# Performance work log

Hardware: AMD Instinct MI355X
Metric: run time of the kernel (lower is better)

Reference implementation:

```python
import jax, jax.numpy as jnp
import numpy as np

N, E, G, L = 100000, 1600000, 2000, 2000
IN, H1, H2, H3, OUT = 128, 64, 32, 16, 16
EPS = 1e-5


def _layernorm(x, g, b):
    m = jnp.mean(x, axis=-1, keepdims=True)
    v = jnp.mean(jnp.square(x - m), axis=-1, keepdims=True)
    return (x - m) * jax.lax.rsqrt(v + EPS) * g + b


def _gcn_block(x, W, b, Wr, br, g, beta, src, dst, deg_inv_sqrt):
    # GCNConv with added self-loops and symmetric normalization (PyG default)
    h = x @ W  # [N, F]
    coef = (deg_inv_sqrt[src] * deg_inv_sqrt[dst])[:, None]  # [E, 1]
    msg = h[src] * coef  # [E, F] -- dominant memory traffic
    agg = jax.ops.segment_sum(msg, dst, num_segments=N)
    agg = agg + h * jnp.square(deg_inv_sqrt)[:, None] + b  # self-loop term + bias
    out = agg + (x @ Wr + br)  # residual projection
    return jax.nn.relu(_layernorm(out, g, beta))


def setup_inputs():
    key = jax.random.key(0)
    ks = jax.random.split(key, 40)
    w = lambda k, i, o: jax.random.normal(k, (i, o), jnp.float32) / np.sqrt(i)
    d = {}
    d['x'] = jax.random.normal(ks[0], (N, IN), jnp.float32)
    d['src'] = jax.random.randint(ks[1], (E,), 0, N, jnp.int32)
    d['dst'] = jax.random.randint(ks[2], (E,), 0, N, jnp.int32)
    d['batch'] = jnp.sort(jax.random.randint(ks[3], (N,), 0, G, jnp.int32))
    d['link_idx'] = jax.random.randint(ks[4], (2, L), 0, G, jnp.int32)
    dims = [(IN, H1), (H1, H2), (H2, H3), (H3, OUT)]
    for i, (fi, fo) in enumerate(dims, 1):
        d[f'W{i}'] = w(ks[5 + 4 * i], fi, fo)
        d[f'b{i}'] = jnp.zeros((fo,), jnp.float32)
        d[f'Wr{i}'] = w(ks[6 + 4 * i], fi, fo)
        d[f'br{i}'] = jnp.zeros((fo,), jnp.float32)
        d[f'g{i}'] = jnp.ones((fo,), jnp.float32)
        d[f'bt{i}'] = jnp.zeros((fo,), jnp.float32)
    d['Wm1'] = w(ks[30], 2 * OUT, OUT)
    d['bm1'] = jnp.zeros((OUT,), jnp.float32)
    d['Wm2'] = w(ks[31], OUT, OUT // 2)
    d['bm2'] = jnp.zeros((OUT // 2,), jnp.float32)
    d['Wm3'] = w(ks[32], OUT // 2, 1)
    d['bm3'] = jnp.zeros((1,), jnp.float32)
    return d


def reference(x, src, dst, batch, link_idx,
              W1, b1, Wr1, br1, g1, bt1,
              W2, b2, Wr2, br2, g2, bt2,
              W3, b3, Wr3, br3, g3, bt3,
              W4, b4, Wr4, br4, g4, bt4,
              Wm1, bm1, Wm2, bm2, Wm3, bm3):
    ones_e = jnp.ones((E,), jnp.float32)
    deg = jax.ops.segment_sum(ones_e, dst, num_segments=N) + 1.0  # + self-loop
    dis = jax.lax.rsqrt(deg)
    h = _gcn_block(x, W1, b1, Wr1, br1, g1, bt1, src, dst, dis)
    h = _gcn_block(h, W2, b2, Wr2, br2, g2, bt2, src, dst, dis)
    h = _gcn_block(h, W3, b3, Wr3, br3, g3, bt3, src, dst, dis)
    h = _gcn_block(h, W4, b4, Wr4, br4, g4, bt4, src, dst, dis)
    # global mean pool over subgraphs
    cnt = jax.ops.segment_sum(jnp.ones((N,), jnp.float32), batch, num_segments=G)
    gemb = jax.ops.segment_sum(h, batch, num_segments=G) / jnp.maximum(cnt, 1.0)[:, None]
    feat = jnp.concatenate([gemb[link_idx[0]], gemb[link_idx[1]]], axis=1)  # [L, 2*OUT]
    z = jax.nn.relu(feat @ Wm1 + bm1)
    z = jax.nn.relu(z @ Wm2 + bm2)
    z = z @ Wm3 + bm3
    return jax.nn.sigmoid(z).squeeze(-1)  # [L]
```

## Files before the change

### kernel.cpp

```cpp
#include <hip/hip_runtime.h>
#include <math.h>

namespace {

constexpr int N = 100000;
constexpr int E = 1600000;
constexpr int G = 2000;
constexpr int L = 2000;

constexpr int SCAN_CHUNK = 1024;
constexpr int NB = (N + SCAN_CHUNK - 1) / SCAN_CHUNK;

constexpr int NXCD = 8;
constexpr int NP = N / NXCD;

__device__ __forceinline__ float bf2f(unsigned short u) {
  union { unsigned int i; float f; } v;
  v.i = ((unsigned int)u) << 16;
  return v.f;
}
__device__ __forceinline__ unsigned short f2bf(float f) {
  union { float f; unsigned int i; } v;
  v.f = f;
  const unsigned int x = v.i;
  return (unsigned short)((x + 0x7FFFu + ((x >> 16) & 1u)) >> 16);
}


__global__ void hist_part_kernel(const int* __restrict__ dst, int* __restrict__ deg) {
  const int part = blockIdx.x & (NXCD - 1);
  const int lo = part * NP;
  const int hi = lo + NP;
  const int bidp = blockIdx.x >> 3;
  const int stridev = (gridDim.x >> 3) * blockDim.x;
  const int nvec = E >> 2;
  for (int v = bidp * blockDim.x + threadIdx.x; v < nvec; v += stridev) {
    const int4 d4 = *reinterpret_cast<const int4*>(dst + v * 4);
    if (d4.x >= lo && d4.x < hi) atomicAdd(&deg[d4.x], 1);
    if (d4.y >= lo && d4.y < hi) atomicAdd(&deg[d4.y], 1);
    if (d4.z >= lo && d4.z < hi) atomicAdd(&deg[d4.z], 1);
    if (d4.w >= lo && d4.w < hi) atomicAdd(&deg[d4.w], 1);
  }
}

__global__ void fill_part_kernel(const int* __restrict__ src, const int* __restrict__ dst,
                                 int* __restrict__ cursor, int* __restrict__ col) {
  const int part = blockIdx.x & (NXCD - 1);
  const int lo = part * NP;
  const int hi = lo + NP;
  const int bidp = blockIdx.x >> 3;
  const int stridev = (gridDim.x >> 3) * blockDim.x;
  const int nvec = E >> 2;
  for (int v = bidp * blockDim.x + threadIdx.x; v < nvec; v += stridev) {
    const int e = v * 4;
    const int4 d4 = *reinterpret_cast<const int4*>(dst + e);
    if (d4.x >= lo && d4.x < hi) col[atomicAdd(&cursor[d4.x], 1)] = src[e];
    if (d4.y >= lo && d4.y < hi) col[atomicAdd(&cursor[d4.y], 1)] = src[e + 1];
    if (d4.z >= lo && d4.z < hi) col[atomicAdd(&cursor[d4.z], 1)] = src[e + 2];
    if (d4.w >= lo && d4.w < hi) col[atomicAdd(&cursor[d4.w], 1)] = src[e + 3];
  }
}

__global__ void scan1_kernel(const int* __restrict__ deg, int* __restrict__ bsum) {
  const int t = threadIdx.x;
  const int base = blockIdx.x * SCAN_CHUNK + t * 4;
  int s = 0;
  if (base < N) {
    const int4 v = *reinterpret_cast<const int4*>(deg + base);
    s = v.x + v.y + v.z + v.w;
  }
  __shared__ int ss[256];
  ss[t] = s;
  __syncthreads();
#pragma unroll
  for (int off = 128; off >= 1; off >>= 1) {
    if (t < off) ss[t] += ss[t + off];
    __syncthreads();
  }
  if (t == 0) bsum[blockIdx.x] = ss[0];
}

__global__ void scan2_kernel(const int* __restrict__ bsum, int* __restrict__ boff) {
  __shared__ int ss[128];
  const int t = threadIdx.x;
  ss[t] = (t < NB) ? bsum[t] : 0;
  __syncthreads();
#pragma unroll
  for (int off = 1; off < 128; off <<= 1) {
    int v = (t >= off) ? ss[t - off] : 0;
    __syncthreads();
    ss[t] += v;
    __syncthreads();
  }
  if (t < NB) boff[t] = (t == 0) ? 0 : ss[t - 1];
}

__global__ void scan3_kernel(const int* __restrict__ deg, const int* __restrict__ boff,
                             int* __restrict__ row_ptr, int* __restrict__ cursor,
                             float* __restrict__ dis) {
  const int t = threadIdx.x;
  const int base = blockIdx.x * SCAN_CHUNK + t * 4;
  int d0 = 0, d1 = 0, d2 = 0, d3 = 0;
  if (base < N) {
    const int4 v = *reinterpret_cast<const int4*>(deg + base);
    d0 = v.x; d1 = v.y; d2 = v.z; d3 = v.w;
  }
  const int tsum = d0 + d1 + d2 + d3;
  __shared__ int ss[256];
  ss[t] = tsum;
  __syncthreads();
#pragma unroll
  for (int off = 1; off < 256; off <<= 1) {
    int v = (t >= off) ? ss[t - off] : 0;
    __syncthreads();
    ss[t] += v;
    __syncthreads();
  }
  if (base < N) {
    const int p0 = ((t == 0) ? 0 : ss[t - 1]) + boff[blockIdx.x];
    const int p1 = p0 + d0;
    const int p2 = p1 + d1;
    const int p3 = p2 + d2;
    *reinterpret_cast<int4*>(row_ptr + base) = make_int4(p0, p1, p2, p3);
    *reinterpret_cast<int4*>(cursor + base) = make_int4(p0, p1, p2, p3);
    const float4 dv = make_float4(rsqrtf((float)d0 + 1.0f), rsqrtf((float)d1 + 1.0f),
                                  rsqrtf((float)d2 + 1.0f), rsqrtf((float)d3 + 1.0f));
    *reinterpret_cast<float4*>(dis + base) = dv;
  }
  if (blockIdx.x == 0 && t == 0) row_ptr[N] = E;
}


__device__ __forceinline__ void f4fma(float4& a, float s, const float4 w) {
  a.x = fmaf(s, w.x, a.x);
  a.y = fmaf(s, w.y, a.y);
  a.z = fmaf(s, w.z, a.z);
  a.w = fmaf(s, w.w, a.w);
}

template <int FI, int FO>
__global__ __launch_bounds__(1024) void gemm2_kernel(const float* __restrict__ x,
                                                     const float* __restrict__ W,
                                                     const float* __restrict__ Wr,
                                                     const float* __restrict__ dis,
                                                     unsigned short* __restrict__ hdb,
                                                     float* __restrict__ r) {
  __shared__ float sW[FI * FO];
  __shared__ float sWr[FI * FO];
  for (int i = threadIdx.x; i < FI * FO; i += blockDim.x) {
    sW[i] = W[i];
    sWr[i] = Wr[i];
  }
  __syncthreads();
  constexpr int CG = FO / 4;
  const int total = (N / 4) * CG;
  const int stride = gridDim.x * blockDim.x;
  for (int idx = blockIdx.x * blockDim.x + threadIdx.x; idx < total; idx += stride) {
    const int rb = idx / CG;
    const int col = (idx - rb * CG) * 4;
    const int row0 = rb * 4;
    float4 aH[4], aR[4];
#pragma unroll
    for (int i = 0; i < 4; ++i) {
      aH[i] = make_float4(0.f, 0.f, 0.f, 0.f);
      aR[i] = make_float4(0.f, 0.f, 0.f, 0.f);
    }
    const float* xr = x + (size_t)row0 * FI;
#pragma unroll
    for (int k = 0; k < FI; k += 4) {
      float xs[4][4];
#pragma unroll
      for (int i = 0; i < 4; ++i) {
        const float4 xv = *reinterpret_cast<const float4*>(xr + i * FI + k);
        xs[i][0] = xv.x; xs[i][1] = xv.y; xs[i][2] = xv.z; xs[i][3] = xv.w;
      }
#pragma unroll
      for (int kk = 0; kk < 4; ++kk) {
        const float4 w4 = *reinterpret_cast<const float4*>(&sW[(k + kk) * FO + col]);
        const float4 w4r = *reinterpret_cast<const float4*>(&sWr[(k + kk) * FO + col]);
#pragma unroll
        for (int i = 0; i < 4; ++i) {
          f4fma(aH[i], xs[i][kk], w4);
          f4fma(aR[i], xs[i][kk], w4r);
        }
      }
    }
    const float4 dv = *reinterpret_cast<const float4*>(dis + row0);
    const float dl[4] = {dv.x, dv.y, dv.z, dv.w};
#pragma unroll
    for (int i = 0; i < 4; ++i) {
      ushort4 ob;
      ob.x = f2bf(aH[i].x * dl[i]);
      ob.y = f2bf(aH[i].y * dl[i]);
      ob.z = f2bf(aH[i].z * dl[i]);
      ob.w = f2bf(aH[i].w * dl[i]);
      *reinterpret_cast<ushort4*>(&hdb[(size_t)(row0 + i) * FO + col]) = ob;
      *reinterpret_cast<float4*>(&r[(size_t)(row0 + i) * FO + col]) = aR[i];
    }
  }
}


template <int FO, bool POOL>
__global__ void gcn_agg_kernel(const int* __restrict__ row_ptr, const int* __restrict__ col,
                               const unsigned short* __restrict__ hdb, const float* __restrict__ r,
                               const float* __restrict__ dis,
                               const float* __restrict__ b, const float* __restrict__ br,
                               const float* __restrict__ g, const float* __restrict__ bt,
                               float* __restrict__ out, const int* __restrict__ batch,
                               float* __restrict__ gemb, float* __restrict__ cnt) {
  constexpr int NPW = 64 / FO;
  const int lane = threadIdx.x & 63;
  const int f = lane & (FO - 1);
  const int sub = lane / FO;
  const int waveId = (blockIdx.x * blockDim.x + threadIdx.x) >> 6;
  const int nWaves = (gridDim.x * blockDim.x) >> 6;
  const int nGroups = N / NPW;
  const float bf = b[f], brf = br[f], gf = g[f], btf = bt[f];
  for (int w = waveId; w < nGroups; w += nWaves) {
    const int node = w * NPW + sub;
    const int beg = row_ptr[node];
    const int end = row_ptr[node + 1];
    float a0 = 0.f, a1 = 0.f, a2 = 0.f, a3 = 0.f;
    int k = beg;
    const int end4 = beg + ((end - beg) & ~3);
    for (; k < end4; k += 4) {
      const int s0 = col[k];
      const int s1 = col[k + 1];
      const int s2 = col[k + 2];
      const int s3 = col[k + 3];
      a0 += bf2f(hdb[(size_t)s0 * FO + f]);
      a1 += bf2f(hdb[(size_t)s1 * FO + f]);
      a2 += bf2f(hdb[(size_t)s2 * FO + f]);
      a3 += bf2f(hdb[(size_t)s3 * FO + f]);
    }
    for (; k < end; ++k) a0 += bf2f(hdb[(size_t)col[k] * FO + f]);
    const float acc = (a0 + a1) + (a2 + a3);
    const float dv = dis[node];
    const size_t base = (size_t)node * FO + f;
    const float v = fmaf(dv, acc + bf2f(hdb[base]), bf + r[base] + brf);
    float s = v;
#pragma unroll
    for (int m = FO / 2; m >= 1; m >>= 1) s += __shfl_xor(s, m, 64);
    const float mean = s * (1.0f / FO);
    const float d0 = v - mean;
    float vs = d0 * d0;
#pragma unroll
    for (int m = FO / 2; m >= 1; m >>= 1) vs += __shfl_xor(vs, m, 64);
    const float var = vs * (1.0f / FO);
    float o = d0 * rsqrtf(var + 1e-5f) * gf + btf;
    o = fmaxf(o, 0.f);
    if (POOL) {
      const int bb = batch[node];
      atomicAdd(&gemb[bb * FO + f], o);
      if (f == 0) atomicAdd(&cnt[bb], 1.0f);
    } else {
      out[base] = o;
    }
  }
}


__global__ void gdiv_kernel(float* __restrict__ gemb, const float* __restrict__ cnt) {
  const int idx = blockIdx.x * blockDim.x + threadIdx.x;
  if (idx < G * 16) gemb[idx] /= fmaxf(cnt[idx >> 4], 1.0f);
}

__global__ void mlp_kernel(const float* __restrict__ gemb, const int* __restrict__ link,
                           const float* __restrict__ Wm1, const float* __restrict__ bm1,
                           const float* __restrict__ Wm2, const float* __restrict__ bm2,
                           const float* __restrict__ Wm3, const float* __restrict__ bm3,
                           float* __restrict__ out) {
  __shared__ float sW1[32 * 16], sW2[16 * 8], sW3[8], sb1[16], sb2[8], sb3;
  for (int i = threadIdx.x; i < 32 * 16; i += blockDim.x) sW1[i] = Wm1[i];
  for (int i = threadIdx.x; i < 16 * 8; i += blockDim.x) sW2[i] = Wm2[i];
  if (threadIdx.x < 8) {
    sW3[threadIdx.x] = Wm3[threadIdx.x];
    sb2[threadIdx.x] = bm2[threadIdx.x];
  }
  if (threadIdx.x < 16) sb1[threadIdx.x] = bm1[threadIdx.x];
  if (threadIdx.x == 0) sb3 = bm3[0];
  __syncthreads();
  const int l = blockIdx.x * blockDim.x + threadIdx.x;
  if (l >= L) return;
  const int a = link[l];
  const int c = link[L + l];
  float feat[32];
#pragma unroll
  for (int k = 0; k < 16; ++k) feat[k] = gemb[a * 16 + k];
#pragma unroll
  for (int k = 0; k < 16; ++k) feat[16 + k] = gemb[c * 16 + k];
  float z1[16];
#pragma unroll
  for (int j = 0; j < 16; ++j) {
    float s = sb1[j];
#pragma unroll
    for (int k = 0; k < 32; ++k) s = fmaf(feat[k], sW1[k * 16 + j], s);
    z1[j] = fmaxf(s, 0.f);
  }
  float z2[8];
#pragma unroll
  for (int j = 0; j < 8; ++j) {
    float s = sb2[j];
#pragma unroll
    for (int k = 0; k < 16; ++k) s = fmaf(z1[k], sW2[k * 8 + j], s);
    z2[j] = fmaxf(s, 0.f);
  }
  float z3 = sb3;
#pragma unroll
  for (int k = 0; k < 8; ++k) z3 = fmaf(z2[k], sW3[k], z3);
  out[l] = 1.f / (1.f + expf(-z3));
}

}

extern "C" void kernel_launch(void* const* d_in, const int* in_sizes, int n_in,
                              void* d_out, int out_size, void* d_ws, size_t ws_size,
                              hipStream_t stream) {
  (void)in_sizes; (void)n_in; (void)out_size; (void)ws_size;
  const float* x = (const float*)d_in[0];
  const int* src = (const int*)d_in[1];
  const int* dst = (const int*)d_in[2];
  const int* batch = (const int*)d_in[3];
  const int* link = (const int*)d_in[4];
  const float *Wl[4], *bl[4], *Wrl[4], *brl[4], *gl[4], *btl[4];
  for (int i = 0; i < 4; ++i) {
    Wl[i] = (const float*)d_in[5 + 6 * i + 0];
    bl[i] = (const float*)d_in[5 + 6 * i + 1];
    Wrl[i] = (const float*)d_in[5 + 6 * i + 2];
    brl[i] = (const float*)d_in[5 + 6 * i + 3];
    gl[i] = (const float*)d_in[5 + 6 * i + 4];
    btl[i] = (const float*)d_in[5 + 6 * i + 5];
  }
  const float* Wm1 = (const float*)d_in[29];
  const float* bm1 = (const float*)d_in[30];
  const float* Wm2 = (const float*)d_in[31];
  const float* bm2 = (const float*)d_in[32];
  const float* Wm3 = (const float*)d_in[33];
  const float* bm3 = (const float*)d_in[34];
  float* out = (float*)d_out;

  char* wsb = (char*)d_ws;
  int* deg_i = (int*)wsb;
  int* row_ptr = deg_i + N;
  int* cursor = row_ptr + (N + 1);
  float* dis = (float*)(cursor + N);
  int* bsum = (int*)(dis + N);
  int* boff = bsum + NB;
  int* col = boff + NB;
  unsigned short* hdb = (unsigned short*)(col + E);
  float* bufB = (float*)(hdb + (size_t)N * 64);
  float* bufC = bufB + (size_t)N * 64;
  float* gemb = bufC + (size_t)N * 64;
  float* cnt = gemb + (size_t)G * 16;

  hipMemsetAsync(deg_i, 0, N * sizeof(int), stream);
  hist_part_kernel<<<2048, 256, 0, stream>>>(dst, deg_i);
  scan1_kernel<<<NB, 256, 0, stream>>>(deg_i, bsum);
  scan2_kernel<<<1, 128, 0, stream>>>(bsum, boff);
  scan3_kernel<<<NB, 256, 0, stream>>>(deg_i, boff, row_ptr, cursor, dis);
  fill_part_kernel<<<2048, 256, 0, stream>>>(src, dst, cursor, col);

  const int AGG_BLOCKS = 2048;

  gemm2_kernel<128, 64><<<((N / 4) * 16 + 1023) / 1024, 1024, 0, stream>>>(x, Wl[0], Wrl[0], dis, hdb, bufB);
  gcn_agg_kernel<64, false><<<AGG_BLOCKS, 256, 0, stream>>>(row_ptr, col, hdb, bufB, dis,
                                                            bl[0], brl[0], gl[0], btl[0], bufC,
                                                            batch, gemb, cnt);
  gemm2_kernel<64, 32><<<((N / 4) * 8 + 1023) / 1024, 1024, 0, stream>>>(bufC, Wl[1], Wrl[1], dis, hdb, bufB);
  gcn_agg_kernel<32, false><<<AGG_BLOCKS, 256, 0, stream>>>(row_ptr, col, hdb, bufB, dis,
                                                            bl[1], brl[1], gl[1], btl[1], bufC,
                                                            batch, gemb, cnt);
  gemm2_kernel<32, 16><<<((N / 4) * 4 + 1023) / 1024, 1024, 0, stream>>>(bufC, Wl[2], Wrl[2], dis, hdb, bufB);
  gcn_agg_kernel<16, false><<<AGG_BLOCKS, 256, 0, stream>>>(row_ptr, col, hdb, bufB, dis,
                                                            bl[2], brl[2], gl[2], btl[2], bufC,
                                                            batch, gemb, cnt);
  hipMemsetAsync(gemb, 0, (size_t)(G * 16 + G) * sizeof(float), stream);
  gemm2_kernel<16, 16><<<((N / 4) * 4 + 1023) / 1024, 1024, 0, stream>>>(bufC, Wl[3], Wrl[3], dis, hdb, bufB);
  gcn_agg_kernel<16, true><<<AGG_BLOCKS, 256, 0, stream>>>(row_ptr, col, hdb, bufB, dis,
                                                           bl[3], brl[3], gl[3], btl[3], nullptr,
                                                           batch, gemb, cnt);
  gdiv_kernel<<<(G * 16 + 255) / 256, 256, 0, stream>>>(gemb, cnt);
  mlp_kernel<<<(L + 255) / 256, 256, 0, stream>>>(gemb, link, Wm1, bm1, Wm2, bm2, Wm3, bm3, out);
}
```

Before: 628.3 us.

## Fuse whole GCN pipeline into one cooperative persistent kernel with grid syncs

Replaces the sequence of about fifteen separate kernel launches and memsets (CSR build, scans, per-layer GEMM and aggregation, pooling divide, MLP) with a single cooperative kernel. Stages are separated by grid.sync(), which removes launch gaps and tail effects between stages. The GEMM now reads weights straight from global memory instead of staging them in LDS, the aggregation loop is unrolled to 8 edges, and the mean-pool division is folded into the MLP. Grid syncs cost time and the grid is capped at 1024 blocks of 256 threads, so phases such as the 1024-thread GEMM and the 2048-block aggregation get less parallelism than before.

```diff
diff --git a/kernel.cpp b/kernel.cpp
--- a/kernel.cpp
+++ b/kernel.cpp
@@ -1,5 +1,8 @@
 #include <hip/hip_runtime.h>
+#include <hip/hip_cooperative_groups.h>
 #include <math.h>
+
+namespace cg = cooperative_groups;
 
 namespace {
 
@@ -26,138 +29,32 @@
   return (unsigned short)((x + 0x7FFFu + ((x >> 16) & 1u)) >> 16);
 }
 
-
-__global__ void hist_part_kernel(const int* __restrict__ dst, int* __restrict__ deg) {
-  const int part = blockIdx.x & (NXCD - 1);
-  const int lo = part * NP;
-  const int hi = lo + NP;
-  const int bidp = blockIdx.x >> 3;
-  const int stridev = (gridDim.x >> 3) * blockDim.x;
-  const int nvec = E >> 2;
-  for (int v = bidp * blockDim.x + threadIdx.x; v < nvec; v += stridev) {
-    const int4 d4 = *reinterpret_cast<const int4*>(dst + v * 4);
-    if (d4.x >= lo && d4.x < hi) atomicAdd(&deg[d4.x], 1);
-    if (d4.y >= lo && d4.y < hi) atomicAdd(&deg[d4.y], 1);
-    if (d4.z >= lo && d4.z < hi) atomicAdd(&deg[d4.z], 1);
-    if (d4.w >= lo && d4.w < hi) atomicAdd(&deg[d4.w], 1);
-  }
-}
-
-__global__ void fill_part_kernel(const int* __restrict__ src, const int* __restrict__ dst,
-                                 int* __restrict__ cursor, int* __restrict__ col) {
-  const int part = blockIdx.x & (NXCD - 1);
-  const int lo = part * NP;
-  const int hi = lo + NP;
-  const int bidp = blockIdx.x >> 3;
-  const int stridev = (gridDim.x >> 3) * blockDim.x;
-  const int nvec = E >> 2;
-  for (int v = bidp * blockDim.x + threadIdx.x; v < nvec; v += stridev) {
-    const int e = v * 4;
-    const int4 d4 = *reinterpret_cast<const int4*>(dst + e);
-    if (d4.x >= lo && d4.x < hi) col[atomicAdd(&cursor[d4.x], 1)] = src[e];
-    if (d4.y >= lo && d4.y < hi) col[atomicAdd(&cursor[d4.y], 1)] = src[e + 1];
-    if (d4.z >= lo && d4.z < hi) col[atomicAdd(&cursor[d4.z], 1)] = src[e + 2];
-    if (d4.w >= lo && d4.w < hi) col[atomicAdd(&cursor[d4.w], 1)] = src[e + 3];
-  }
-}
-
-__global__ void scan1_kernel(const int* __restrict__ deg, int* __restrict__ bsum) {
-  const int t = threadIdx.x;
-  const int base = blockIdx.x * SCAN_CHUNK + t * 4;
-  int s = 0;
-  if (base < N) {
-    const int4 v = *reinterpret_cast<const int4*>(deg + base);
-    s = v.x + v.y + v.z + v.w;
-  }
-  __shared__ int ss[256];
-  ss[t] = s;
-  __syncthreads();
-#pragma unroll
-  for (int off = 128; off >= 1; off >>= 1) {
-    if (t < off) ss[t] += ss[t + off];
-    __syncthreads();
-  }
-  if (t == 0) bsum[blockIdx.x] = ss[0];
-}
-
-__global__ void scan2_kernel(const int* __restrict__ bsum, int* __restrict__ boff) {
-  __shared__ int ss[128];
-  const int t = threadIdx.x;
-  ss[t] = (t < NB) ? bsum[t] : 0;
-  __syncthreads();
-#pragma unroll
-  for (int off = 1; off < 128; off <<= 1) {
-    int v = (t >= off) ? ss[t - off] : 0;
-    __syncthreads();
-    ss[t] += v;
-    __syncthreads();
-  }
-  if (t < NB) boff[t] = (t == 0) ? 0 : ss[t - 1];
-}
-
-__global__ void scan3_kernel(const int* __restrict__ deg, const int* __restrict__ boff,
-                             int* __restrict__ row_ptr, int* __restrict__ cursor,
-                             float* __restrict__ dis) {
-  const int t = threadIdx.x;
-  const int base = blockIdx.x * SCAN_CHUNK + t * 4;
-  int d0 = 0, d1 = 0, d2 = 0, d3 = 0;
-  if (base < N) {
-    const int4 v = *reinterpret_cast<const int4*>(deg + base);
-    d0 = v.x; d1 = v.y; d2 = v.z; d3 = v.w;
-  }
-  const int tsum = d0 + d1 + d2 + d3;
-  __shared__ int ss[256];
-  ss[t] = tsum;
-  __syncthreads();
-#pragma unroll
-  for (int off = 1; off < 256; off <<= 1) {
-    int v = (t >= off) ? ss[t - off] : 0;
-    __syncthreads();
-    ss[t] += v;
-    __syncthreads();
-  }
-  if (base < N) {
-    const int p0 = ((t == 0) ? 0 : ss[t - 1]) + boff[blockIdx.x];
-    const int p1 = p0 + d0;
-    const int p2 = p1 + d1;
-    const int p3 = p2 + d2;
-    *reinterpret_cast<int4*>(row_ptr + base) = make_int4(p0, p1, p2, p3);
-    *reinterpret_cast<int4*>(cursor + base) = make_int4(p0, p1, p2, p3);
-    const float4 dv = make_float4(rsqrtf((float)d0 + 1.0f), rsqrtf((float)d1 + 1.0f),
-                                  rsqrtf((float)d2 + 1.0f), rsqrtf((float)d3 + 1.0f));
-    *reinterpret_cast<float4*>(dis + base) = dv;
-  }
-  if (blockIdx.x == 0 && t == 0) row_ptr[N] = E;
-}
-
-
-__device__ __forceinline__ void f4fma(float4& a, float s, const float4 w) {
-  a.x = fmaf(s, w.x, a.x);
-  a.y = fmaf(s, w.y, a.y);
-  a.z = fmaf(s, w.z, a.z);
-  a.w = fmaf(s, w.w, a.w);
-}
+struct Params {
+  const float* x;
+  const int* src; const int* dst; const int* batch; const int* link;
+  const float* W[4]; const float* b[4]; const float* Wr[4]; const float* br[4];
+  const float* g[4]; const float* bt[4];
+  const float* Wm1; const float* bm1; const float* Wm2; const float* bm2;
+  const float* Wm3; const float* bm3;
+  float* out;
+  int* deg; int* row_ptr; int* cursor; float* dis;
+  int* bsum; int* boff; int* col;
+  unsigned short* hdb;
+  float* r;
+  float* io;
+  float* gemb; float* cnt;
+};
 
 template <int FI, int FO>
-__global__ __launch_bounds__(1024) void gemm2_kernel(const float* __restrict__ x,
-                                                     const float* __restrict__ W,
-                                                     const float* __restrict__ Wr,
-                                                     const float* __restrict__ dis,
-                                                     unsigned short* __restrict__ hdb,
-                                                     float* __restrict__ r) {
-  __shared__ float sW[FI * FO];
-  __shared__ float sWr[FI * FO];
-  for (int i = threadIdx.x; i < FI * FO; i += blockDim.x) {
-    sW[i] = W[i];
-    sWr[i] = Wr[i];
-  }
-  __syncthreads();
+__device__ void gemm_phase(const float* __restrict__ xin, const float* __restrict__ W,
+                           const float* __restrict__ Wr, const float* __restrict__ dis,
+                           unsigned short* __restrict__ hdb, float* __restrict__ r,
+                           int gtid, int gsz) {
   constexpr int CG = FO / 4;
   const int total = (N / 4) * CG;
-  const int stride = gridDim.x * blockDim.x;
-  for (int idx = blockIdx.x * blockDim.x + threadIdx.x; idx < total; idx += stride) {
+  for (int idx = gtid; idx < total; idx += gsz) {
     const int rb = idx / CG;
-    const int col = (idx - rb * CG) * 4;
+    const int colq = (idx - rb * CG) * 4;
     const int row0 = rb * 4;
     float4 aH[4], aR[4];
 #pragma unroll
@@ -165,7 +62,7 @@
       aH[i] = make_float4(0.f, 0.f, 0.f, 0.f);
       aR[i] = make_float4(0.f, 0.f, 0.f, 0.f);
     }
-    const float* xr = x + (size_t)row0 * FI;
+    const float* xr = xin + (size_t)row0 * FI;
 #pragma unroll
     for (int k = 0; k < FI; k += 4) {
       float xs[4][4];
@@ -176,12 +73,18 @@
       }
 #pragma unroll
       for (int kk = 0; kk < 4; ++kk) {
-        const float4 w4 = *reinterpret_cast<const float4*>(&sW[(k + kk) * FO + col]);
-        const float4 w4r = *reinterpret_cast<const float4*>(&sWr[(k + kk) * FO + col]);
+        const float4 w4 = *reinterpret_cast<const float4*>(&W[(k + kk) * FO + colq]);
+        const float4 w4r = *reinterpret_cast<const float4*>(&Wr[(k + kk) * FO + colq]);
 #pragma unroll
         for (int i = 0; i < 4; ++i) {
-          f4fma(aH[i], xs[i][kk], w4);
-          f4fma(aR[i], xs[i][kk], w4r);
+          aH[i].x = fmaf(xs[i][kk], w4.x, aH[i].x);
+          aH[i].y = fmaf(xs[i][kk], w4.y, aH[i].y);
+          aH[i].z = fmaf(xs[i][kk], w4.z, aH[i].z);
+          aH[i].w = fmaf(xs[i][kk], w4.w, aH[i].w);
+          aR[i].x = fmaf(xs[i][kk], w4r.x, aR[i].x);
+          aR[i].y = fmaf(xs[i][kk], w4r.y, aR[i].y);
+          aR[i].z = fmaf(xs[i][kk], w4r.z, aR[i].z);
+          aR[i].w = fmaf(xs[i][kk], w4r.w, aR[i].w);
         }
       }
     }
@@ -194,48 +97,56 @@
       ob.y = f2bf(aH[i].y * dl[i]);
       ob.z = f2bf(aH[i].z * dl[i]);
       ob.w = f2bf(aH[i].w * dl[i]);
-      *reinterpret_cast<ushort4*>(&hdb[(size_t)(row0 + i) * FO + col]) = ob;
-      *reinterpret_cast<float4*>(&r[(size_t)(row0 + i) * FO + col]) = aR[i];
-    }
-  }
-}
-
+      *reinterpret_cast<ushort4*>(&hdb[(size_t)(row0 + i) * FO + colq]) = ob;
+      *reinterpret_cast<float4*>(&r[(size_t)(row0 + i) * FO + colq]) = aR[i];
+    }
+  }
+}
 
 template <int FO, bool POOL>
-__global__ void gcn_agg_kernel(const int* __restrict__ row_ptr, const int* __restrict__ col,
-                               const unsigned short* __restrict__ hdb, const float* __restrict__ r,
-                               const float* __restrict__ dis,
-                               const float* __restrict__ b, const float* __restrict__ br,
-                               const float* __restrict__ g, const float* __restrict__ bt,
-                               float* __restrict__ out, const int* __restrict__ batch,
-                               float* __restrict__ gemb, float* __restrict__ cnt) {
+__device__ void agg_phase(const int* __restrict__ row_ptr, const int* __restrict__ col,
+                          const unsigned short* __restrict__ hdb, const float* __restrict__ r,
+                          const float* __restrict__ dis,
+                          const float* __restrict__ b, const float* __restrict__ br,
+                          const float* __restrict__ g, const float* __restrict__ bt,
+                          float* __restrict__ out, const int* __restrict__ batch,
+                          float* __restrict__ gemb, float* __restrict__ cnt,
+                          int gtid, int gsz) {
   constexpr int NPW = 64 / FO;
-  const int lane = threadIdx.x & 63;
+  const int lane = gtid & 63;
   const int f = lane & (FO - 1);
   const int sub = lane / FO;
-  const int waveId = (blockIdx.x * blockDim.x + threadIdx.x) >> 6;
-  const int nWaves = (gridDim.x * blockDim.x) >> 6;
+  const int waveId = gtid >> 6;
+  const int nWaves = gsz >> 6;
   const int nGroups = N / NPW;
   const float bf = b[f], brf = br[f], gf = g[f], btf = bt[f];
   for (int w = waveId; w < nGroups; w += nWaves) {
     const int node = w * NPW + sub;
     const int beg = row_ptr[node];
     const int end = row_ptr[node + 1];
-    float a0 = 0.f, a1 = 0.f, a2 = 0.f, a3 = 0.f;
+    float a0 = 0.f, a1 = 0.f, a2 = 0.f, a3 = 0.f, a4 = 0.f, a5 = 0.f, a6 = 0.f, a7 = 0.f;
     int k = beg;
-    const int end4 = beg + ((end - beg) & ~3);
-    for (; k < end4; k += 4) {
+    const int end8 = beg + ((end - beg) & ~7);
+    for (; k < end8; k += 8) {
       const int s0 = col[k];
       const int s1 = col[k + 1];
       const int s2 = col[k + 2];
       const int s3 = col[k + 3];
+      const int s4 = col[k + 4];
+      const int s5 = col[k + 5];
+      const int s6 = col[k + 6];
+      const int s7 = col[k + 7];
       a0 += bf2f(hdb[(size_t)s0 * FO + f]);
       a1 += bf2f(hdb[(size_t)s1 * FO + f]);
       a2 += bf2f(hdb[(size_t)s2 * FO + f]);
       a3 += bf2f(hdb[(size_t)s3 * FO + f]);
+      a4 += bf2f(hdb[(size_t)s4 * FO + f]);
+      a5 += bf2f(hdb[(size_t)s5 * FO + f]);
+      a6 += bf2f(hdb[(size_t)s6 * FO + f]);
+      a7 += bf2f(hdb[(size_t)s7 * FO + f]);
     }
     for (; k < end; ++k) a0 += bf2f(hdb[(size_t)col[k] * FO + f]);
-    const float acc = (a0 + a1) + (a2 + a3);
+    const float acc = ((a0 + a1) + (a2 + a3)) + ((a4 + a5) + (a6 + a7));
     const float dv = dis[node];
     const size_t base = (size_t)node * FO + f;
     const float v = fmaf(dv, acc + bf2f(hdb[base]), bf + r[base] + brf);
@@ -260,56 +171,177 @@
   }
 }
 
-
-__global__ void gdiv_kernel(float* __restrict__ gemb, const float* __restrict__ cnt) {
-  const int idx = blockIdx.x * blockDim.x + threadIdx.x;
-  if (idx < G * 16) gemb[idx] /= fmaxf(cnt[idx >> 4], 1.0f);
-}
-
-__global__ void mlp_kernel(const float* __restrict__ gemb, const int* __restrict__ link,
-                           const float* __restrict__ Wm1, const float* __restrict__ bm1,
-                           const float* __restrict__ Wm2, const float* __restrict__ bm2,
-                           const float* __restrict__ Wm3, const float* __restrict__ bm3,
-                           float* __restrict__ out) {
-  __shared__ float sW1[32 * 16], sW2[16 * 8], sW3[8], sb1[16], sb2[8], sb3;
-  for (int i = threadIdx.x; i < 32 * 16; i += blockDim.x) sW1[i] = Wm1[i];
-  for (int i = threadIdx.x; i < 16 * 8; i += blockDim.x) sW2[i] = Wm2[i];
-  if (threadIdx.x < 8) {
-    sW3[threadIdx.x] = Wm3[threadIdx.x];
-    sb2[threadIdx.x] = bm2[threadIdx.x];
-  }
-  if (threadIdx.x < 16) sb1[threadIdx.x] = bm1[threadIdx.x];
-  if (threadIdx.x == 0) sb3 = bm3[0];
-  __syncthreads();
-  const int l = blockIdx.x * blockDim.x + threadIdx.x;
-  if (l >= L) return;
-  const int a = link[l];
-  const int c = link[L + l];
-  float feat[32];
-#pragma unroll
-  for (int k = 0; k < 16; ++k) feat[k] = gemb[a * 16 + k];
-#pragma unroll
-  for (int k = 0; k < 16; ++k) feat[16 + k] = gemb[c * 16 + k];
-  float z1[16];
-#pragma unroll
-  for (int j = 0; j < 16; ++j) {
-    float s = sb1[j];
-#pragma unroll
-    for (int k = 0; k < 32; ++k) s = fmaf(feat[k], sW1[k * 16 + j], s);
-    z1[j] = fmaxf(s, 0.f);
-  }
-  float z2[8];
-#pragma unroll
-  for (int j = 0; j < 8; ++j) {
-    float s = sb2[j];
-#pragma unroll
-    for (int k = 0; k < 16; ++k) s = fmaf(z1[k], sW2[k * 8 + j], s);
-    z2[j] = fmaxf(s, 0.f);
-  }
-  float z3 = sb3;
-#pragma unroll
-  for (int k = 0; k < 8; ++k) z3 = fmaf(z2[k], sW3[k], z3);
-  out[l] = 1.f / (1.f + expf(-z3));
+__global__ __launch_bounds__(256, 4) void fused_kernel(Params p) {
+  cg::grid_group grid = cg::this_grid();
+  const int tid = threadIdx.x;
+  const int bid = blockIdx.x;
+  const int gtid = bid * blockDim.x + tid;
+  const int gsz = gridDim.x * blockDim.x;
+
+  for (int i = gtid; i < N; i += gsz) p.deg[i] = 0;
+  for (int i = gtid; i < G * 16; i += gsz) p.gemb[i] = 0.f;
+  for (int i = gtid; i < G; i += gsz) p.cnt[i] = 0.f;
+  grid.sync();
+
+  {
+    const int part = bid & (NXCD - 1);
+    const int lo = part * NP;
+    const int hi = lo + NP;
+    const int bidp = bid >> 3;
+    const int stridev = (gridDim.x >> 3) * blockDim.x;
+    const int nvec = E >> 2;
+    for (int v = bidp * blockDim.x + tid; v < nvec; v += stridev) {
+      const int4 d4 = *reinterpret_cast<const int4*>(p.dst + v * 4);
+      if (d4.x >= lo && d4.x < hi) atomicAdd(&p.deg[d4.x], 1);
+      if (d4.y >= lo && d4.y < hi) atomicAdd(&p.deg[d4.y], 1);
+      if (d4.z >= lo && d4.z < hi) atomicAdd(&p.deg[d4.z], 1);
+      if (d4.w >= lo && d4.w < hi) atomicAdd(&p.deg[d4.w], 1);
+    }
+  }
+  grid.sync();
+
+  {
+    __shared__ int ss1[256];
+    if (bid < NB) {
+      const int base = bid * SCAN_CHUNK + tid * 4;
+      int s = 0;
+      if (base < N) {
+        const int4 v = *reinterpret_cast<const int4*>(p.deg + base);
+        s = v.x + v.y + v.z + v.w;
+      }
+      ss1[tid] = s;
+      __syncthreads();
+#pragma unroll
+      for (int off = 128; off >= 1; off >>= 1) {
+        if (tid < off) ss1[tid] += ss1[tid + off];
+        __syncthreads();
+      }
+      if (tid == 0) p.bsum[bid] = ss1[0];
+    }
+  }
+  grid.sync();
+
+  {
+    __shared__ int ss2[256];
+    if (bid == 0) {
+      ss2[tid] = (tid < NB) ? p.bsum[tid] : 0;
+      __syncthreads();
+#pragma unroll
+      for (int off = 1; off < 256; off <<= 1) {
+        const int v = (tid >= off) ? ss2[tid - off] : 0;
+        __syncthreads();
+        ss2[tid] += v;
+        __syncthreads();
+      }
+      if (tid < NB) p.boff[tid] = (tid == 0) ? 0 : ss2[tid - 1];
+    }
+  }
+  grid.sync();
+
+  {
+    __shared__ int ss3[256];
+    if (bid < NB) {
+      const int base = bid * SCAN_CHUNK + tid * 4;
+      int d0 = 0, d1 = 0, d2 = 0, d3 = 0;
+      if (base < N) {
+        const int4 v = *reinterpret_cast<const int4*>(p.deg + base);
+        d0 = v.x; d1 = v.y; d2 = v.z; d3 = v.w;
+      }
+      ss3[tid] = d0 + d1 + d2 + d3;
+      __syncthreads();
+#pragma unroll
+      for (int off = 1; off < 256; off <<= 1) {
+        const int v = (tid >= off) ? ss3[tid - off] : 0;
+        __syncthreads();
+        ss3[tid] += v;
+        __syncthreads();
+      }
+      if (base < N) {
+        const int p0 = ((tid == 0) ? 0 : ss3[tid - 1]) + p.boff[bid];
+        const int p1 = p0 + d0;
+        const int p2 = p1 + d1;
+        const int p3 = p2 + d2;
+        *reinterpret_cast<int4*>(p.row_ptr + base) = make_int4(p0, p1, p2, p3);
+        *reinterpret_cast<int4*>(p.cursor + base) = make_int4(p0, p1, p2, p3);
+        const float4 dv = make_float4(rsqrtf((float)d0 + 1.0f), rsqrtf((float)d1 + 1.0f),
+                                      rsqrtf((float)d2 + 1.0f), rsqrtf((float)d3 + 1.0f));
+        *reinterpret_cast<float4*>(p.dis + base) = dv;
+      }
+      if (bid == 0 && tid == 0) p.row_ptr[N] = E;
+    }
+  }
+  grid.sync();
+
+  {
+    const int part = bid & (NXCD - 1);
+    const int lo = part * NP;
+    const int hi = lo + NP;
+    const int bidp = bid >> 3;
+    const int stridev = (gridDim.x >> 3) * blockDim.x;
+    const int nvec = E >> 2;
+    for (int v = bidp * blockDim.x + tid; v < nvec; v += stridev) {
+      const int e = v * 4;
+      const int4 d4 = *reinterpret_cast<const int4*>(p.dst + e);
+      if (d4.x >= lo && d4.x < hi) p.col[atomicAdd(&p.cursor[d4.x], 1)] = p.src[e];
+      if (d4.y >= lo && d4.y < hi) p.col[atomicAdd(&p.cursor[d4.y], 1)] = p.src[e + 1];
+      if (d4.z >= lo && d4.z < hi) p.col[atomicAdd(&p.cursor[d4.z], 1)] = p.src[e + 2];
+      if (d4.w >= lo && d4.w < hi) p.col[atomicAdd(&p.cursor[d4.w], 1)] = p.src[e + 3];
+    }
+  }
+  grid.sync();
+
+  gemm_phase<128, 64>(p.x, p.W[0], p.Wr[0], p.dis, p.hdb, p.r, gtid, gsz);
+  grid.sync();
+  agg_phase<64, false>(p.row_ptr, p.col, p.hdb, p.r, p.dis, p.b[0], p.br[0], p.g[0], p.bt[0],
+                       p.io, p.batch, p.gemb, p.cnt, gtid, gsz);
+  grid.sync();
+  gemm_phase<64, 32>(p.io, p.W[1], p.Wr[1], p.dis, p.hdb, p.r, gtid, gsz);
+  grid.sync();
+  agg_phase<32, false>(p.row_ptr, p.col, p.hdb, p.r, p.dis, p.b[1], p.br[1], p.g[1], p.bt[1],
+                       p.io, p.batch, p.gemb, p.cnt, gtid, gsz);
+  grid.sync();
+  gemm_phase<32, 16>(p.io, p.W[2], p.Wr[2], p.dis, p.hdb, p.r, gtid, gsz);
+  grid.sync();
+  agg_phase<16, false>(p.row_ptr, p.col, p.hdb, p.r, p.dis, p.b[2], p.br[2], p.g[2], p.bt[2],
+                       p.io, p.batch, p.gemb, p.cnt, gtid, gsz);
+  grid.sync();
+  gemm_phase<16, 16>(p.io, p.W[3], p.Wr[3], p.dis, p.hdb, p.r, gtid, gsz);
+  grid.sync();
+  agg_phase<16, true>(p.row_ptr, p.col, p.hdb, p.r, p.dis, p.b[3], p.br[3], p.g[3], p.bt[3],
+                      nullptr, p.batch, p.gemb, p.cnt, gtid, gsz);
+  grid.sync();
+
+  if (gtid < L) {
+    const int a = p.link[gtid];
+    const int c = p.link[L + gtid];
+    const float ia = 1.0f / fmaxf(p.cnt[a], 1.0f);
+    const float ic = 1.0f / fmaxf(p.cnt[c], 1.0f);
+    float feat[32];
+#pragma unroll
+    for (int k = 0; k < 16; ++k) feat[k] = p.gemb[a * 16 + k] * ia;
+#pragma unroll
+    for (int k = 0; k < 16; ++k) feat[16 + k] = p.gemb[c * 16 + k] * ic;
+    float z1[16];
+#pragma unroll
+    for (int j = 0; j < 16; ++j) {
+      float s = p.bm1[j];
+#pragma unroll
+      for (int k = 0; k < 32; ++k) s = fmaf(feat[k], p.Wm1[k * 16 + j], s);
+      z1[j] = fmaxf(s, 0.f);
+    }
+    float z2[8];
+#pragma unroll
+    for (int j = 0; j < 8; ++j) {
+      float s = p.bm2[j];
+#pragma unroll
+      for (int k = 0; k < 16; ++k) s = fmaf(z1[k], p.Wm2[k * 8 + j], s);
+      z2[j] = fmaxf(s, 0.f);
+    }
+    float z3 = p.bm3[0];
+#pragma unroll
+    for (int k = 0; k < 8; ++k) z3 = fmaf(z2[k], p.Wm3[k], z3);
+    p.out[gtid] = 1.f / (1.f + expf(-z3));
+  }
 }
 
 }
@@ -318,68 +350,51 @@
                               void* d_out, int out_size, void* d_ws, size_t ws_size,
                               hipStream_t stream) {
   (void)in_sizes; (void)n_in; (void)out_size; (void)ws_size;
-  const float* x = (const float*)d_in[0];
-  const int* src = (const int*)d_in[1];
-  const int* dst = (const int*)d_in[2];
-  const int* batch = (const int*)d_in[3];
-  const int* link = (const int*)d_in[4];
-  const float *Wl[4], *bl[4], *Wrl[4], *brl[4], *gl[4], *btl[4];
+  Params p;
+  p.x = (const float*)d_in[0];
+  p.src = (const int*)d_in[1];
+  p.dst = (const int*)d_in[2];
+  p.batch = (const int*)d_in[3];
+  p.link = (const int*)d_in[4];
   for (int i = 0; i < 4; ++i) {
-    Wl[i] = (const float*)d_in[5 + 6 * i + 0];
-    bl[i] = (const float*)d_in[5 + 6 * i + 1];
-    Wrl[i] = (const float*)d_in[5 + 6 * i + 2];
-    brl[i] = (const float*)d_in[5 + 6 * i + 3];
-    gl[i] = (const float*)d_in[5 + 6 * i + 4];
-    btl[i] = (const float*)d_in[5 + 6 * i + 5];
-  }
-  const float* Wm1 = (const float*)d_in[29];
-  const float* bm1 = (const float*)d_in[30];
-  const float* Wm2 = (const float*)d_in[31];
-  const float* bm2 = (const float*)d_in[32];
-  const float* Wm3 = (const float*)d_in[33];
-  const float* bm3 = (const float*)d_in[34];
-  float* out = (float*)d_out;
+    p.W[i] = (const float*)d_in[5 + 6 * i + 0];
+    p.b[i] = (const float*)d_in[5 + 6 * i + 1];
+    p.Wr[i] = (const float*)d_in[5 + 6 * i + 2];
+    p.br[i] = (const float*)d_in[5 + 6 * i + 3];
+    p.g[i] = (const float*)d_in[5 + 6 * i + 4];
+    p.bt[i] = (const float*)d_in[5 + 6 * i + 5];
+  }
+  p.Wm1 = (const float*)d_in[29];
+  p.bm1 = (const float*)d_in[30];
+  p.Wm2 = (const float*)d_in[31];
+  p.bm2 = (const float*)d_in[32];
+  p.Wm3 = (const float*)d_in[33];
+  p.bm3 = (const float*)d_in[34];
+  p.out = (float*)d_out;
 
   char* wsb = (char*)d_ws;
-  int* deg_i = (int*)wsb;
-  int* row_ptr = deg_i + N;
-  int* cursor = row_ptr + (N + 1);
-  float* dis = (float*)(cursor + N);
-  int* bsum = (int*)(dis + N);
-  int* boff = bsum + NB;
-  int* col = boff + NB;
-  unsigned short* hdb = (unsigned short*)(col + E);
-  float* bufB = (float*)(hdb + (size_t)N * 64);
-  float* bufC = bufB + (size_t)N * 64;
-  float* gemb = bufC + (size_t)N * 64;
-  float* cnt = gemb + (size_t)G * 16;
-
-  hipMemsetAsync(deg_i, 0, N * sizeof(int), stream);
-  hist_part_kernel<<<2048, 256, 0, stream>>>(dst, deg_i);
-  scan1_kernel<<<NB, 256, 0, stream>>>(deg_i, bsum);
-  scan2_kernel<<<1, 128, 0, stream>>>(bsum, boff);
-  scan3_kernel<<<NB, 256, 0, stream>>>(deg_i, boff, row_ptr, cursor, dis);
-  fill_part_kernel<<<2048, 256, 0, stream>>>(src, dst, cursor, col);
-
-  const int AGG_BLOCKS = 2048;
-
-  gemm2_kernel<128, 64><<<((N / 4) * 16 + 1023) / 1024, 1024, 0, stream>>>(x, Wl[0], Wrl[0], dis, hdb, bufB);
-  gcn_agg_kernel<64, false><<<AGG_BLOCKS, 256, 0, stream>>>(row_ptr, col, hdb, bufB, dis,
-                                                            bl[0], brl[0], gl[0], btl[0], bufC,
-                                                            batch, gemb, cnt);
-  gemm2_kernel<64, 32><<<((N / 4) * 8 + 1023) / 1024, 1024, 0, stream>>>(bufC, Wl[1], Wrl[1], dis, hdb, bufB);
-  gcn_agg_kernel<32, false><<<AGG_BLOCKS, 256, 0, stream>>>(row_ptr, col, hdb, bufB, dis,
-                                                            bl[1], brl[1], gl[1], btl[1], bufC,
-                                                            batch, gemb, cnt);
-  gemm2_kernel<32, 16><<<((N / 4) * 4 + 1023) / 1024, 1024, 0, stream>>>(bufC, Wl[2], Wrl[2], dis, hdb, bufB);
-  gcn_agg_kernel<16, false><<<AGG_BLOCKS, 256, 0, stream>>>(row_ptr, col, hdb, bufB, dis,
-                                                            bl[2], brl[2], gl[2], btl[2], bufC,
-                                                            batch, gemb, cnt);
-  hipMemsetAsync(gemb, 0, (size_t)(G * 16 + G) * sizeof(float), stream);
-  gemm2_kernel<16, 16><<<((N / 4) * 4 + 1023) / 1024, 1024, 0, stream>>>(bufC, Wl[3], Wrl[3], dis, hdb, bufB);
-  gcn_agg_kernel<16, true><<<AGG_BLOCKS, 256, 0, stream>>>(row_ptr, col, hdb, bufB, dis,
-                                                           bl[3], brl[3], gl[3], btl[3], nullptr,
-                                                           batch, gemb, cnt);
-  gdiv_kernel<<<(G * 16 + 255) / 256, 256, 0, stream>>>(gemb, cnt);
-  mlp_kernel<<<(L + 255) / 256, 256, 0, stream>>>(gemb, link, Wm1, bm1, Wm2, bm2, Wm3, bm3, out);
-}
+  p.deg = (int*)wsb;
+  p.row_ptr = p.deg + N;
+  p.cursor = p.row_ptr + (N + 1);
+  p.dis = (float*)(p.cursor + N);
+  p.bsum = (int*)(p.dis + N);
+  p.boff = p.bsum + NB;
+  p.col = p.boff + NB;
+  p.hdb = (unsigned short*)(p.col + E);
+  p.r = (float*)(p.hdb + (size_t)N * 64);
+  p.io = p.r + (size_t)N * 64;
+  p.gemb = p.io + (size_t)N * 64;
+  p.cnt = p.gemb + (size_t)G * 16;
+
+  int maxBlocksPerCU = 0;
+  hipOccupancyMaxActiveBlocksPerMultiprocessor(&maxBlocksPerCU, fused_kernel, 256, 0);
+  if (maxBlocksPerCU <= 0) maxBlocksPerCU = 3;
+  long long blocks = (long long)maxBlocksPerCU * 256;
+  if (blocks > 1024) blocks = 1024;
+  blocks &= ~7LL;
+  if (blocks < 104) blocks = 104;
+
+  void* args[] = {&p};
+  hipLaunchCooperativeKernel((void*)fused_kernel, dim3((unsigned)blocks), dim3(256), args, 0,
+                             stream);
+}
```

Measured after the change: 1.770 ms. 182% more time.
